# Kernel optimization log

Hardware: AMD Instinct MI355X
Metric: run time of the kernel (lower is better)

Reference implementation:

```python
import jax, jax.numpy as jnp
import numpy as np

B, H, L, D, MODES = 8, 8, 4096, 64, 64
SCALE = D ** -0.5  # (d_model // n_heads) ** -0.5


def setup_inputs() -> dict:
    key = jax.random.key(0)
    kq, kk, kv = jax.random.split(key, 3)
    q = jax.random.normal(kq, (B, H, L, D), dtype=jnp.float32)
    k = jax.random.normal(kk, (B, H, L, D), dtype=jnp.float32)
    v = jax.random.normal(kv, (B, H, L, D), dtype=jnp.float32)
    # unique sorted frequency-mode indices in [0, L//2), like get_frequency_modes
    rng = np.random.default_rng(0)
    idx_q = jnp.asarray(np.sort(rng.choice(L // 2, MODES, replace=False)), dtype=jnp.int32)
    idx_k = jnp.asarray(np.sort(rng.choice(L // 2, MODES, replace=False)), dtype=jnp.int32)
    idx_v = jnp.asarray(np.sort(rng.choice(L // 2, MODES, replace=False)), dtype=jnp.int32)
    return {"q": q, "k": k, "v": v, "idx_q": idx_q, "idx_k": idx_k, "idx_v": idx_v}


def reference(q, k, v, idx_q, idx_k, idx_v):
    L_ = q.shape[2]
    # rFFT over sequence axis, then gather selected frequency modes (vectorized gather,
    # replacing the python per-index slice-assignment loop in the original)
    q_ft = jnp.fft.rfft(q, axis=2)[:, :, idx_q, :]  # [B,H,M,D] complex64
    k_ft = jnp.fft.rfft(k, axis=2)[:, :, idx_k, :]
    v_ft = jnp.fft.rfft(v, axis=2)[:, :, idx_v, :]
    # complex attention over modes; no conjugation (torch.matmul semantics)
    qk_ft = jnp.einsum('bhmd,bhnd->bhmn', q_ft, k_ft) * SCALE
    scores = jnp.tanh(qk_ft)  # complex tanh, matching torch
    values = jnp.einsum('bhmn,bhnd->bhmd', scores, v_ft)  # [B,H,M,D]
    # irfft treats the M modes as the first frequency bins, zero-padded to L//2+1
    out = jnp.fft.irfft(values, n=L_, axis=2)  # [B,H,L,D] real
    return out
```

## Files before the change

kernel.cpp:

```cpp
#include <hip/hip_runtime.h>
#include <hip/hip_bf16.h>
#include <math.h>

#define LSEQ 4096
#define DIM 64
#define TWO_PI 6.28318530717958647692f

typedef __attribute__((ext_vector_type(8))) short bf16x8;
typedef __attribute__((ext_vector_type(4))) float f32x4;


__device__ __forceinline__ unsigned short f2bfu(float f) {
  __hip_bfloat16 h = __float2bfloat16(f);
  return *(unsigned short*)&h;
}
__device__ __forceinline__ float bfu2f(unsigned short h) {
  union { unsigned int u; float f; } z;
  z.u = ((unsigned int)h) << 16;
  return z.f;
}

__global__ __launch_bounds__(256) void init_btT(unsigned short* __restrict__ btT) {
  int u = blockIdx.x * 256 + threadIdx.x;
  int l = u >> 7, kk = u & 127;
  int f = kk >> 1;
  float ang = (float)((f * l) & 4095) * (TWO_PI / 4096.0f);
  float s, c;
  sincosf(ang, &s, &c);
  float val = (kk & 1) ? -s : c;
  btT[u] = f2bfu(val);
}

__global__ __launch_bounds__(256) void init_w(unsigned short* __restrict__ whi,
                                              unsigned short* __restrict__ wlo,
                                              const int* __restrict__ iq,
                                              const int* __restrict__ ik,
                                              const int* __restrict__ iv) {
  int u = blockIdx.x * 256 + threadIdx.x;
  int tensor = u >> 19;
  int rem = u & 524287;
  int row = rem >> 12;
  int l = rem & 4095;
  int m = row & 63, reim = row >> 6;
  const int* idx = (tensor == 0 ? iq : tensor == 1 ? ik : iv);
  int f = idx[m];
  float ang = (float)((f * l) & 4095) * (TWO_PI / 4096.0f);
  float s, c;
  sincosf(ang, &s, &c);
  float val = reim ? -s : c;
  __hip_bfloat16 hb = __float2bfloat16(val);
  float fh = __bfloat162float(hb);
  whi[u] = *(unsigned short*)&hb;
  wlo[u] = f2bfu(val - fh);
}

__global__ __launch_bounds__(256) void dft_mfma(
    const float* __restrict__ q, const float* __restrict__ k,
    const float* __restrict__ v, const unsigned short* __restrict__ whi,
    const unsigned short* __restrict__ wlo, float* __restrict__ ftQK,
    unsigned short* __restrict__ ftV) {
  int b = blockIdx.x;
  int tensor = b >> 8;
  int bh = (b >> 2) & 63;
  int part = b & 3;
  const float* x =
      (tensor == 0 ? q : tensor == 1 ? k : v) + (size_t)bh * (LSEQ * DIM);
  const unsigned short* wh = whi + (size_t)tensor * 524288;
  const unsigned short* wl = wlo + (size_t)tensor * 524288;

  int t = threadIdx.x;
  int lane = t & 63, w = t >> 6;
  int l15 = lane & 15, qd = lane >> 4;
  int xd = t & 63, xseg = t >> 6;

  __shared__ __align__(16) unsigned short Xh[2][64 * 72];
  __shared__ __align__(16) unsigned short Xl[2][64 * 72];

  f32x4 acc[2][4];
#pragma unroll
  for (int mt = 0; mt < 2; ++mt)
#pragma unroll
    for (int nt = 0; nt < 4; ++nt) acc[mt][nt] = (f32x4){0.f, 0.f, 0.f, 0.f};

  bool split = (tensor != 2);
  int k0 = part * 1024;

  int rowA = w * 32 + l15;
  int rowB = rowA + 16;
  const unsigned short* wrh0 = wh + (size_t)rowA * 4096 + qd * 8;
  const unsigned short* wrh1 = wh + (size_t)rowB * 4096 + qd * 8;
  const unsigned short* wrl0 = wl + (size_t)rowA * 4096 + qd * 8;
  const unsigned short* wrl1 = wl + (size_t)rowB * 4096 + qd * 8;

  float xv[16];

  auto cvstore = [&](int buf) {
    __align__(16) unsigned short hs[16];
    __align__(16) unsigned short ls[16];
#pragma unroll
    for (int i = 0; i < 16; ++i) {
      __hip_bfloat16 hb = __float2bfloat16(xv[i]);
      hs[i] = *(unsigned short*)&hb;
      float fh = __bfloat162float(hb);
      ls[i] = f2bfu(xv[i] - fh);
    }
    *(bf16x8*)&Xh[buf][xd * 72 + xseg * 16] = *(bf16x8*)&hs[0];
    *(bf16x8*)&Xh[buf][xd * 72 + xseg * 16 + 8] = *(bf16x8*)&hs[8];
    *(bf16x8*)&Xl[buf][xd * 72 + xseg * 16] = *(bf16x8*)&ls[0];
    *(bf16x8*)&Xl[buf][xd * 72 + xseg * 16 + 8] = *(bf16x8*)&ls[8];
  };

  {
    const float* xp = x + (size_t)(k0 + xseg * 16) * 64 + xd;
#pragma unroll
    for (int i = 0; i < 16; ++i) xv[i] = xp[(size_t)i * 64];
  }
  cvstore(0);

#pragma unroll 2
  for (int ch = 0; ch < 16; ++ch) {
    int lc = k0 + ch * 64;
    int cur = ch & 1;

    bf16x8 afh[2][2], afl[2][2];
#pragma unroll
    for (int ks = 0; ks < 2; ++ks) {
      afh[0][ks] = *(const bf16x8*)(wrh0 + lc + ks * 32);
      afh[1][ks] = *(const bf16x8*)(wrh1 + lc + ks * 32);
    }
    if (split) {
#pragma unroll
      for (int ks = 0; ks < 2; ++ks) {
        afl[0][ks] = *(const bf16x8*)(wrl0 + lc + ks * 32);
        afl[1][ks] = *(const bf16x8*)(wrl1 + lc + ks * 32);
      }
    }

    if (ch < 15) {
      const float* xp = x + (size_t)(lc + 64 + xseg * 16) * 64 + xd;
#pragma unroll
      for (int i = 0; i < 16; ++i) xv[i] = xp[(size_t)i * 64];
    }

    __syncthreads();

    if (split) {
#pragma unroll
      for (int ks = 0; ks < 2; ++ks) {
        bf16x8 bh_[4], bl_[4];
#pragma unroll
        for (int nt = 0; nt < 4; ++nt) {
          bh_[nt] =
              *(const bf16x8*)&Xh[cur][(nt * 16 + l15) * 72 + ks * 32 + qd * 8];
          bl_[nt] =
              *(const bf16x8*)&Xl[cur][(nt * 16 + l15) * 72 + ks * 32 + qd * 8];
        }
#pragma unroll
        for (int mt = 0; mt < 2; ++mt)
#pragma unroll
          for (int nt = 0; nt < 4; ++nt) {
            acc[mt][nt] = __builtin_amdgcn_mfma_f32_16x16x32_bf16(
                afh[mt][ks], bh_[nt], acc[mt][nt], 0, 0, 0);
            acc[mt][nt] = __builtin_amdgcn_mfma_f32_16x16x32_bf16(
                afh[mt][ks], bl_[nt], acc[mt][nt], 0, 0, 0);
            acc[mt][nt] = __builtin_amdgcn_mfma_f32_16x16x32_bf16(
                afl[mt][ks], bh_[nt], acc[mt][nt], 0, 0, 0);
          }
      }
    } else {
#pragma unroll
      for (int ks = 0; ks < 2; ++ks) {
        bf16x8 bh_[4], bl_[4];
#pragma unroll
        for (int nt = 0; nt < 4; ++nt) {
          bh_[nt] =
              *(const bf16x8*)&Xh[cur][(nt * 16 + l15) * 72 + ks * 32 + qd * 8];
          bl_[nt] =
              *(const bf16x8*)&Xl[cur][(nt * 16 + l15) * 72 + ks * 32 + qd * 8];
        }
#pragma unroll
        for (int mt = 0; mt < 2; ++mt)
#pragma unroll
          for (int nt = 0; nt < 4; ++nt) {
            acc[mt][nt] = __builtin_amdgcn_mfma_f32_16x16x32_bf16(
                afh[mt][ks], bh_[nt], acc[mt][nt], 0, 0, 0);
            acc[mt][nt] = __builtin_amdgcn_mfma_f32_16x16x32_bf16(
                afh[mt][ks], bl_[nt], acc[mt][nt], 0, 0, 0);
          }
      }
    }

    if (ch < 15) cvstore(cur ^ 1);
  }

  if (tensor < 2) {
    float* o = ftQK + ((size_t)(tensor * 64 + bh) * 4 + part) * 8192;
#pragma unroll
    for (int mt = 0; mt < 2; ++mt) {
      int row0 = (w * 2 + mt) * 16 + qd * 4;
#pragma unroll
      for (int nt = 0; nt < 4; ++nt) {
        int col = nt * 16 + l15;
#pragma unroll
        for (int r = 0; r < 4; ++r) o[(row0 + r) * 64 + col] = acc[mt][nt][r];
      }
    }
  } else {
    unsigned short* o = ftV + ((size_t)bh * 4 + part) * 8192;
#pragma unroll
    for (int mt = 0; mt < 2; ++mt) {
      int row0 = (w * 2 + mt) * 16 + qd * 4;
#pragma unroll
      for (int nt = 0; nt < 4; ++nt) {
        int col = nt * 16 + l15;
#pragma unroll
        for (int r = 0; r < 4; ++r)
          o[(row0 + r) * 64 + col] = f2bfu(acc[mt][nt][r]);
      }
    }
  }
}

#define FST 132
__global__ __launch_bounds__(256) void attn(const float* __restrict__ ftQK,
                                            const unsigned short* __restrict__ ftV,
                                            unsigned short* __restrict__ ypt) {
  int bh = blockIdx.x >> 2, mq = blockIdx.x & 3;
  int t = threadIdx.x;

  __shared__ float qf[16 * FST];
  __shared__ float kf[64 * FST];
  __shared__ float vf[64 * FST];
  __shared__ float S[16 * FST];

  const float* qb = ftQK + (size_t)bh * 4 * 8192;
  const float* kb = ftQK + (size_t)(64 + bh) * 4 * 8192;
  const unsigned short* vb = ftV + (size_t)bh * 4 * 8192;

#pragma unroll
  for (int j = 0; j < 8; ++j) {
    int u4 = t + 256 * j;
    int row = u4 >> 4, dq = u4 & 15;
    float4 ksum = make_float4(0.f, 0.f, 0.f, 0.f);
    float vsum[4] = {0.f, 0.f, 0.f, 0.f};
#pragma unroll
    for (int p = 0; p < 4; ++p) {
      float4 a = *(const float4*)&kb[(size_t)p * 8192 + row * 64 + dq * 4];
      ksum.x += a.x; ksum.y += a.y; ksum.z += a.z; ksum.w += a.w;
      ushort4 vv = *(const ushort4*)&vb[(size_t)p * 8192 + row * 64 + dq * 4];
      vsum[0] += bfu2f(vv.x); vsum[1] += bfu2f(vv.y);
      vsum[2] += bfu2f(vv.z); vsum[3] += bfu2f(vv.w);
    }
    int mm = row & 63, reim = row >> 6;
    int base = mm * FST + reim;
    kf[base + 2 * (4 * dq + 0)] = ksum.x;
    kf[base + 2 * (4 * dq + 1)] = ksum.y;
    kf[base + 2 * (4 * dq + 2)] = ksum.z;
    kf[base + 2 * (4 * dq + 3)] = ksum.w;
    vf[base + 2 * (4 * dq + 0)] = vsum[0];
    vf[base + 2 * (4 * dq + 1)] = vsum[1];
    vf[base + 2 * (4 * dq + 2)] = vsum[2];
    vf[base + 2 * (4 * dq + 3)] = vsum[3];
  }
#pragma unroll
  for (int j = 0; j < 2; ++j) {
    int u4 = t + 256 * j;
    int rl = u4 >> 4, dq = u4 & 15;
    int i = rl & 15, reim = rl >> 4;
    int row = reim * 64 + mq * 16 + i;
    float4 qsum = make_float4(0.f, 0.f, 0.f, 0.f);
#pragma unroll
    for (int p = 0; p < 4; ++p) {
      float4 a = *(const float4*)&qb[(size_t)p * 8192 + row * 64 + dq * 4];
      qsum.x += a.x; qsum.y += a.y; qsum.z += a.z; qsum.w += a.w;
    }
    int base = i * FST + reim;
    qf[base + 2 * (4 * dq + 0)] = qsum.x;
    qf[base + 2 * (4 * dq + 1)] = qsum.y;
    qf[base + 2 * (4 * dq + 2)] = qsum.z;
    qf[base + 2 * (4 * dq + 3)] = qsum.w;
  }
  __syncthreads();

  int m = t >> 4;
  int n0 = t & 15;
#pragma unroll
  for (int nn = 0; nn < 4; ++nn) {
    int n = n0 + 16 * nn;
    float xr = 0.0f, xi = 0.0f;
    for (int d2 = 0; d2 < 32; ++d2) {
      float4 qv = *(const float4*)&qf[m * FST + 4 * d2];
      float4 kv = *(const float4*)&kf[n * FST + 4 * d2];
      xr = fmaf(qv.x, kv.x, xr); xr = fmaf(-qv.y, kv.y, xr);
      xi = fmaf(qv.x, kv.y, xi); xi = fmaf(qv.y, kv.x, xi);
      xr = fmaf(qv.z, kv.z, xr); xr = fmaf(-qv.w, kv.w, xr);
      xi = fmaf(qv.z, kv.w, xi); xi = fmaf(qv.w, kv.z, xi);
    }
    float x = xr * 0.125f, y = xi * 0.125f;
    float tr, tim;
    if (fabsf(x) > 40.0f) {
      tr = x > 0.0f ? 1.0f : -1.0f;
      tim = 0.0f;
    } else {
      float sh = sinhf(2.0f * x), ch = coshf(2.0f * x);
      float sn, cn;
      sincosf(2.0f * y, &sn, &cn);
      float den = ch + cn;
      tr = sh / den;
      tim = sn / den;
    }
    S[m * FST + 2 * n] = tr;
    S[m * FST + 2 * n + 1] = tim;
  }
  __syncthreads();

  int d0 = t & 15;
  float ar4[4] = {0, 0, 0, 0}, ai4[4] = {0, 0, 0, 0};
  for (int n = 0; n < 64; ++n) {
    float sr_ = S[m * FST + 2 * n];
    float si_ = S[m * FST + 2 * n + 1];
    float4 va = *(const float4*)&vf[n * FST + 8 * d0];
    float4 vb2 = *(const float4*)&vf[n * FST + 8 * d0 + 4];
    ar4[0] = fmaf(sr_, va.x, ar4[0]); ar4[0] = fmaf(-si_, va.y, ar4[0]);
    ai4[0] = fmaf(sr_, va.y, ai4[0]); ai4[0] = fmaf(si_, va.x, ai4[0]);
    ar4[1] = fmaf(sr_, va.z, ar4[1]); ar4[1] = fmaf(-si_, va.w, ar4[1]);
    ai4[1] = fmaf(sr_, va.w, ai4[1]); ai4[1] = fmaf(si_, va.z, ai4[1]);
    ar4[2] = fmaf(sr_, vb2.x, ar4[2]); ar4[2] = fmaf(-si_, vb2.y, ar4[2]);
    ai4[2] = fmaf(sr_, vb2.y, ai4[2]); ai4[2] = fmaf(si_, vb2.x, ai4[2]);
    ar4[3] = fmaf(sr_, vb2.z, ar4[3]); ar4[3] = fmaf(-si_, vb2.w, ar4[3]);
    ai4[3] = fmaf(sr_, vb2.w, ai4[3]); ai4[3] = fmaf(si_, vb2.z, ai4[3]);
  }
  int fbin = mq * 16 + m;
  float cf = (fbin == 0 ? 1.0f : 2.0f) / 4096.0f;
#pragma unroll
  for (int c = 0; c < 4; ++c) {
    int d = 4 * d0 + c;
    ypt[((size_t)bh * 64 + d) * 128 + 2 * fbin] = f2bfu(cf * ar4[c]);
    ypt[((size_t)bh * 64 + d) * 128 + 2 * fbin + 1] = f2bfu(cf * ai4[c]);
  }
}

__global__ __launch_bounds__(256) void irfft_mfma(
    const unsigned short* __restrict__ ypt,
    const unsigned short* __restrict__ btT, float* __restrict__ out) {
  int bh = blockIdx.x >> 6, lc = blockIdx.x & 63;
  int t = threadIdx.x;
  int lane = t & 63, w = t >> 6;
  int l15 = lane & 15, qd = lane >> 4;

  __shared__ __align__(16) unsigned short A[2 * 64 * 72];
  __shared__ __align__(16) unsigned short Bm[2 * 64 * 72];

#pragma unroll
  for (int j = 0; j < 4; ++j) {
    int u = t + 256 * j;
    int row = u >> 4, seg = u & 15;
    int kh = seg >> 3, s8 = seg & 7;
    *(float4*)&A[kh * 4608 + row * 72 + s8 * 8] =
        *(const float4*)&btT[(size_t)(lc * 64 + row) * 128 + seg * 8];
    *(float4*)&Bm[kh * 4608 + row * 72 + s8 * 8] =
        *(const float4*)&ypt[(size_t)(bh * 64 + row) * 128 + seg * 8];
  }
  __syncthreads();

  f32x4 acc[4];
#pragma unroll
  for (int nt = 0; nt < 4; ++nt) acc[nt] = (f32x4){0.f, 0.f, 0.f, 0.f};

#pragma unroll
  for (int kh = 0; kh < 2; ++kh)
#pragma unroll
    for (int ks = 0; ks < 2; ++ks) {
      bf16x8 af =
          *(const bf16x8*)&A[kh * 4608 + (w * 16 + l15) * 72 + ks * 32 + qd * 8];
#pragma unroll
      for (int nt = 0; nt < 4; ++nt) {
        bf16x8 bf =
            *(const bf16x8*)&Bm[kh * 4608 + (nt * 16 + l15) * 72 + ks * 32 +
                                qd * 8];
        acc[nt] = __builtin_amdgcn_mfma_f32_16x16x32_bf16(af, bf, acc[nt], 0, 0, 0);
      }
    }

  float* obase = out + ((size_t)bh * 4096 + lc * 64) * 64;
  int row0 = w * 16 + qd * 4;
#pragma unroll
  for (int nt = 0; nt < 4; ++nt) {
    int col = nt * 16 + l15;
#pragma unroll
    for (int r = 0; r < 4; ++r) obase[(row0 + r) * 64 + col] = acc[nt][r];
  }
}

extern "C" void kernel_launch(void* const* d_in, const int* in_sizes, int n_in,
                              void* d_out, int out_size, void* d_ws,
                              size_t ws_size, hipStream_t stream) {
  const float* q = (const float*)d_in[0];
  const float* k = (const float*)d_in[1];
  const float* v = (const float*)d_in[2];
  const int* iq = (const int*)d_in[3];
  const int* ik = (const int*)d_in[4];
  const int* iv = (const int*)d_in[5];
  char* ws = (char*)d_ws;
  unsigned short* btT = (unsigned short*)ws;
  unsigned short* ypt = (unsigned short*)(ws + 1048576);
  float* ftQK = (float*)(ws + 2097152);
  unsigned short* ftV = (unsigned short*)(ws + 18874368);
  unsigned short* whi = (unsigned short*)(ws + 23068672);
  unsigned short* wlo = (unsigned short*)(ws + 26214400);
  float* out = (float*)d_out;

  hipLaunchKernelGGL(init_btT, dim3(2048), dim3(256), 0, stream, btT);
  hipLaunchKernelGGL(init_w, dim3(6144), dim3(256), 0, stream, whi, wlo, iq,
                     ik, iv);
  hipLaunchKernelGGL(dft_mfma, dim3(768), dim3(256), 0, stream, q, k, v, whi,
                     wlo, ftQK, ftV);
  hipLaunchKernelGGL(attn, dim3(256), dim3(256), 0, stream, ftQK, ftV, ypt);
  hipLaunchKernelGGL(irfft_mfma, dim3(4096), dim3(256), 0, stream, ypt, btT,
                     out);
}
```

Measured before the change: 262.5 us.

## Stage DFT twiddle panels into LDS via async global_load_lds with swizzled layout

The twiddle matrices are rewritten at init into 32-column panels with an XOR swizzle. The DFT kernel then streams each panel straight into double-buffered shared memory with global_load_lds, replacing per-lane strided global reads. The K chunk drops from 64 to 32 and the loop becomes a two-stage pipeline with explicit waitcnt and barriers, so X prefetch and panel loads overlap the MFMA work. This relies on hand-tuned vmcnt accounting and doubles the number of barrier iterations.

```diff
diff --git a/kernel.cpp b/kernel.cpp
--- a/kernel.cpp
+++ b/kernel.cpp
@@ -19,6 +19,11 @@
   z.u = ((unsigned int)h) << 16;
   return z.f;
 }
+
+#define GLOAD16(gsrc, ldst)                                              \
+  __builtin_amdgcn_global_load_lds(                                      \
+      (const __attribute__((address_space(1))) void*)(gsrc),             \
+      (__attribute__((address_space(3))) void*)(ldst), 16, 0, 0)
 
 __global__ __launch_bounds__(256) void init_btT(unsigned short* __restrict__ btT) {
   int u = blockIdx.x * 256 + threadIdx.x;
@@ -50,8 +55,11 @@
   float val = reim ? -s : c;
   __hip_bfloat16 hb = __float2bfloat16(val);
   float fh = __bfloat162float(hb);
-  whi[u] = *(unsigned short*)&hb;
-  wlo[u] = f2bfu(val - fh);
+  int panel = l >> 5, kc = l & 31, seg = kc >> 3;
+  int o = (tensor << 19) + (panel << 12) + (row << 5) +
+          (((seg ^ (row & 3)) << 3) | (kc & 7));
+  whi[o] = *(unsigned short*)&hb;
+  wlo[o] = f2bfu(val - fh);
 }
 
 __global__ __launch_bounds__(256) void dft_mfma(
@@ -65,16 +73,18 @@
   int part = b & 3;
   const float* x =
       (tensor == 0 ? q : tensor == 1 ? k : v) + (size_t)bh * (LSEQ * DIM);
-  const unsigned short* wh = whi + (size_t)tensor * 524288;
-  const unsigned short* wl = wlo + (size_t)tensor * 524288;
+  const unsigned short* wph = whi + (size_t)(tensor * 128 + part * 32) * 4096;
+  const unsigned short* wpl = wlo + (size_t)(tensor * 128 + part * 32) * 4096;
 
   int t = threadIdx.x;
   int lane = t & 63, w = t >> 6;
   int l15 = lane & 15, qd = lane >> 4;
   int xd = t & 63, xseg = t >> 6;
 
-  __shared__ __align__(16) unsigned short Xh[2][64 * 72];
-  __shared__ __align__(16) unsigned short Xl[2][64 * 72];
+  __shared__ __align__(16) unsigned short Wh[2][4096];
+  __shared__ __align__(16) unsigned short Wl[2][4096];
+  __shared__ __align__(16) unsigned short Xh[2][64 * 40];
+  __shared__ __align__(16) unsigned short Xl[2][64 * 40];
 
   f32x4 acc[2][4];
 #pragma unroll
@@ -85,112 +95,115 @@
   bool split = (tensor != 2);
   int k0 = part * 1024;
 
-  int rowA = w * 32 + l15;
-  int rowB = rowA + 16;
-  const unsigned short* wrh0 = wh + (size_t)rowA * 4096 + qd * 8;
-  const unsigned short* wrh1 = wh + (size_t)rowB * 4096 + qd * 8;
-  const unsigned short* wrl0 = wl + (size_t)rowA * 4096 + qd * 8;
-  const unsigned short* wrl1 = wl + (size_t)rowB * 4096 + qd * 8;
-
-  float xv[16];
-
-  auto cvstore = [&](int buf) {
-    __align__(16) unsigned short hs[16];
-    __align__(16) unsigned short ls[16];
-#pragma unroll
-    for (int i = 0; i < 16; ++i) {
+  float xvA[8], xvB[8];
+
+  auto cvstore = [&](int buf, float (&xv)[8]) {
+    __align__(16) unsigned short hs[8];
+    __align__(16) unsigned short ls[8];
+#pragma unroll
+    for (int i = 0; i < 8; ++i) {
       __hip_bfloat16 hb = __float2bfloat16(xv[i]);
       hs[i] = *(unsigned short*)&hb;
       float fh = __bfloat162float(hb);
       ls[i] = f2bfu(xv[i] - fh);
     }
-    *(bf16x8*)&Xh[buf][xd * 72 + xseg * 16] = *(bf16x8*)&hs[0];
-    *(bf16x8*)&Xh[buf][xd * 72 + xseg * 16 + 8] = *(bf16x8*)&hs[8];
-    *(bf16x8*)&Xl[buf][xd * 72 + xseg * 16] = *(bf16x8*)&ls[0];
-    *(bf16x8*)&Xl[buf][xd * 72 + xseg * 16 + 8] = *(bf16x8*)&ls[8];
+    *(bf16x8*)&Xh[buf][xd * 40 + xseg * 8] = *(bf16x8*)&hs[0];
+    *(bf16x8*)&Xl[buf][xd * 40 + xseg * 8] = *(bf16x8*)&ls[0];
   };
 
   {
-    const float* xp = x + (size_t)(k0 + xseg * 16) * 64 + xd;
-#pragma unroll
-    for (int i = 0; i < 16; ++i) xv[i] = xp[(size_t)i * 64];
-  }
-  cvstore(0);
-
-#pragma unroll 2
-  for (int ch = 0; ch < 16; ++ch) {
-    int lc = k0 + ch * 64;
-    int cur = ch & 1;
-
-    bf16x8 afh[2][2], afl[2][2];
-#pragma unroll
-    for (int ks = 0; ks < 2; ++ks) {
-      afh[0][ks] = *(const bf16x8*)(wrh0 + lc + ks * 32);
-      afh[1][ks] = *(const bf16x8*)(wrh1 + lc + ks * 32);
-    }
+    GLOAD16(wph + t * 8, &Wh[0][t * 8]);
+    GLOAD16(wph + 2048 + t * 8, &Wh[0][t * 8 + 2048]);
     if (split) {
-#pragma unroll
-      for (int ks = 0; ks < 2; ++ks) {
-        afl[0][ks] = *(const bf16x8*)(wrl0 + lc + ks * 32);
-        afl[1][ks] = *(const bf16x8*)(wrl1 + lc + ks * 32);
+      GLOAD16(wpl + t * 8, &Wl[0][t * 8]);
+      GLOAD16(wpl + 2048 + t * 8, &Wl[0][t * 8 + 2048]);
+    }
+    __builtin_amdgcn_sched_barrier(0);
+    const float* xp = x + (size_t)(k0 + xseg * 8) * 64 + xd;
+#pragma unroll
+    for (int i = 0; i < 8; ++i) xvA[i] = xp[(size_t)i * 64];
+    cvstore(0, xvA);
+    const float* xp1 = x + (size_t)(k0 + 32 + xseg * 8) * 64 + xd;
+#pragma unroll
+    for (int i = 0; i < 8; ++i) xvB[i] = xp1[(size_t)i * 64];
+  }
+
+  auto body = [&](int ch, int cur, float (&xvLoad)[8], float (&xvUse)[8]) {
+    if (ch == 31)
+      asm volatile("s_waitcnt lgkmcnt(0) vmcnt(0)" ::: "memory");
+    else
+      asm volatile("s_waitcnt lgkmcnt(0) vmcnt(8)" ::: "memory");
+    __builtin_amdgcn_s_barrier();
+    __builtin_amdgcn_sched_barrier(0);
+
+    if (ch < 31) {
+      const unsigned short* ph = wph + (size_t)(ch + 1) * 4096 + t * 8;
+      GLOAD16(ph, &Wh[cur ^ 1][t * 8]);
+      GLOAD16(ph + 2048, &Wh[cur ^ 1][t * 8 + 2048]);
+      if (split) {
+        const unsigned short* pl = wpl + (size_t)(ch + 1) * 4096 + t * 8;
+        GLOAD16(pl, &Wl[cur ^ 1][t * 8]);
+        GLOAD16(pl + 2048, &Wl[cur ^ 1][t * 8 + 2048]);
       }
-    }
-
-    if (ch < 15) {
-      const float* xp = x + (size_t)(lc + 64 + xseg * 16) * 64 + xd;
-#pragma unroll
-      for (int i = 0; i < 16; ++i) xv[i] = xp[(size_t)i * 64];
-    }
-
-    __syncthreads();
-
+      __builtin_amdgcn_sched_barrier(0);
+    }
+
+    if (ch < 30) {
+      const float* xp =
+          x + (size_t)(k0 + (ch + 2) * 32 + xseg * 8) * 64 + xd;
+#pragma unroll
+      for (int i = 0; i < 8; ++i) xvLoad[i] = xp[(size_t)i * 64];
+    }
+
+    bf16x8 ah[2], al[2], bh_[4], bl_[4];
+#pragma unroll
+    for (int mt = 0; mt < 2; ++mt) {
+      int row = (w * 2 + mt) * 16 + l15;
+      ah[mt] = *(const bf16x8*)&Wh[cur][row * 32 + ((qd ^ (l15 & 3)) << 3)];
+    }
     if (split) {
 #pragma unroll
-      for (int ks = 0; ks < 2; ++ks) {
-        bf16x8 bh_[4], bl_[4];
+      for (int mt = 0; mt < 2; ++mt) {
+        int row = (w * 2 + mt) * 16 + l15;
+        al[mt] = *(const bf16x8*)&Wl[cur][row * 32 + ((qd ^ (l15 & 3)) << 3)];
+      }
+    }
+#pragma unroll
+    for (int nt = 0; nt < 4; ++nt) {
+      bh_[nt] = *(const bf16x8*)&Xh[cur][(nt * 16 + l15) * 40 + qd * 8];
+      bl_[nt] = *(const bf16x8*)&Xl[cur][(nt * 16 + l15) * 40 + qd * 8];
+    }
+    if (split) {
+#pragma unroll
+      for (int mt = 0; mt < 2; ++mt)
 #pragma unroll
         for (int nt = 0; nt < 4; ++nt) {
-          bh_[nt] =
-              *(const bf16x8*)&Xh[cur][(nt * 16 + l15) * 72 + ks * 32 + qd * 8];
-          bl_[nt] =
-              *(const bf16x8*)&Xl[cur][(nt * 16 + l15) * 72 + ks * 32 + qd * 8];
+          acc[mt][nt] = __builtin_amdgcn_mfma_f32_16x16x32_bf16(
+              ah[mt], bh_[nt], acc[mt][nt], 0, 0, 0);
+          acc[mt][nt] = __builtin_amdgcn_mfma_f32_16x16x32_bf16(
+              ah[mt], bl_[nt], acc[mt][nt], 0, 0, 0);
+          acc[mt][nt] = __builtin_amdgcn_mfma_f32_16x16x32_bf16(
+              al[mt], bh_[nt], acc[mt][nt], 0, 0, 0);
         }
-#pragma unroll
-        for (int mt = 0; mt < 2; ++mt)
-#pragma unroll
-          for (int nt = 0; nt < 4; ++nt) {
-            acc[mt][nt] = __builtin_amdgcn_mfma_f32_16x16x32_bf16(
-                afh[mt][ks], bh_[nt], acc[mt][nt], 0, 0, 0);
-            acc[mt][nt] = __builtin_amdgcn_mfma_f32_16x16x32_bf16(
-                afh[mt][ks], bl_[nt], acc[mt][nt], 0, 0, 0);
-            acc[mt][nt] = __builtin_amdgcn_mfma_f32_16x16x32_bf16(
-                afl[mt][ks], bh_[nt], acc[mt][nt], 0, 0, 0);
-          }
-      }
     } else {
 #pragma unroll
-      for (int ks = 0; ks < 2; ++ks) {
-        bf16x8 bh_[4], bl_[4];
+      for (int mt = 0; mt < 2; ++mt)
 #pragma unroll
         for (int nt = 0; nt < 4; ++nt) {
-          bh_[nt] =
-              *(const bf16x8*)&Xh[cur][(nt * 16 + l15) * 72 + ks * 32 + qd * 8];
-          bl_[nt] =
-              *(const bf16x8*)&Xl[cur][(nt * 16 + l15) * 72 + ks * 32 + qd * 8];
+          acc[mt][nt] = __builtin_amdgcn_mfma_f32_16x16x32_bf16(
+              ah[mt], bh_[nt], acc[mt][nt], 0, 0, 0);
+          acc[mt][nt] = __builtin_amdgcn_mfma_f32_16x16x32_bf16(
+              ah[mt], bl_[nt], acc[mt][nt], 0, 0, 0);
         }
-#pragma unroll
-        for (int mt = 0; mt < 2; ++mt)
-#pragma unroll
-          for (int nt = 0; nt < 4; ++nt) {
-            acc[mt][nt] = __builtin_amdgcn_mfma_f32_16x16x32_bf16(
-                afh[mt][ks], bh_[nt], acc[mt][nt], 0, 0, 0);
-            acc[mt][nt] = __builtin_amdgcn_mfma_f32_16x16x32_bf16(
-                afh[mt][ks], bl_[nt], acc[mt][nt], 0, 0, 0);
-          }
-      }
-    }
-
-    if (ch < 15) cvstore(cur ^ 1);
+    }
+
+    if (ch < 31) cvstore(cur ^ 1, xvUse);
+  };
+
+#pragma unroll 1
+  for (int cc = 0; cc < 16; ++cc) {
+    body(2 * cc, 0, xvA, xvB);
+    body(2 * cc + 1, 1, xvB, xvA);
   }
 
   if (tensor < 2) {
```

Result: faster. 255.9 us (-2.5%).
